# Kernel optimization log

Hardware: AMD Instinct MI355X
Metric: run time of the kernel (lower is better)

Reference implementation:

```python
import jax, jax.numpy as jnp
import numpy as np

B, C, P, H, W = 8, 256, 64, 64, 64


def conv2d(x, w, b, pad):
    y = jax.lax.conv_general_dilated(
        x, w, window_strides=(1, 1), padding=[(pad, pad), (pad, pad)],
        dimension_numbers=("NCHW", "OIHW", "NCHW"))
    return y + b[None, :, None, None]


def setup_inputs() -> dict:
    key = jax.random.key(0)
    ks = jax.random.split(key, 9)
    x = jax.random.normal(ks[0], (B, C, H, W), dtype=jnp.float32)
    # conv weights, OIHW layout; scale ~ kaiming-ish
    w_top = jax.random.normal(ks[1], (P, C, 1, 1), jnp.float32) * (1.0 / np.sqrt(C))
    b_top = jnp.zeros((P,), jnp.float32)
    w_center = jax.random.normal(ks[2], (P, C, 1, 1), jnp.float32) * (1.0 / np.sqrt(C))
    b_center = jnp.zeros((P,), jnp.float32)
    w_bottom = jax.random.normal(ks[3], (C, C, 3, 3), jnp.float32) * (1.0 / np.sqrt(9 * C))
    b_bottom = jnp.zeros((C,), jnp.float32)
    w_out = jax.random.normal(ks[4], (C, C, 3, 3), jnp.float32) * (1.0 / np.sqrt(9 * C))
    b_out = jnp.zeros((C,), jnp.float32)
    return {"x": x, "w_top": w_top, "b_top": b_top, "w_center": w_center,
            "b_center": b_center, "w_bottom": w_bottom, "b_bottom": b_bottom,
            "w_out": w_out, "b_out": b_out}


def reference(x, w_top, b_top, w_center, b_center, w_bottom, b_bottom, w_out, b_out):
    b, c, h, w = x.shape
    hw = h * w
    x_top = conv2d(x, w_top, b_top, 0).reshape(b, -1, hw)          # [B, P, HW]
    x_center = conv2d(x, w_center, b_center, 0).reshape(b, -1, hw)  # [B, P, HW]
    x_center = jnp.swapaxes(x_center, 1, 2)                          # [B, HW, P]
    x_bottom = conv2d(x, w_bottom, b_bottom, 1).reshape(b, c, hw)
    x_bottom = jnp.swapaxes(x_bottom, 1, 2)                          # [B, HW, C]
    sp_map = jnp.einsum("bnp,bpm->bnm", x_center, x_top)            # [B, HW, HW]
    # NOTE: softmax is GLOBAL over the flattened HW*HW map per batch element,
    # not per-row (faithful to original Softmax(dim=1) on view(bsize, -1)).
    sp_map = jax.nn.softmax(sp_map.reshape(b, -1), axis=1).reshape(b, hw, hw)
    sp_map = jnp.einsum("bnm,bmc->bnc", sp_map, x_bottom)           # [B, HW, C]
    # NOTE: original does .reshape(b, C, h, w) on a [B, HW, C] tensor (no
    # transpose) -- replicate that exact memory reinterpretation.
    sp_map = sp_map.reshape(b, c, h, w)
    return conv2d(x + sp_map, w_out, b_out, 1)
```

## Files before the change

kernel.cpp:

```cpp
#include <hip/hip_runtime.h>
#include <hip/hip_bf16.h>
#include <type_traits>

constexpr int B_ = 8, C_ = 256, P_ = 64, H_ = 64, W_ = 64, HW_ = 4096;

typedef __attribute__((ext_vector_type(8))) short short8;
typedef __attribute__((ext_vector_type(4))) short short4v;
typedef __attribute__((ext_vector_type(4))) float f32x4;

__device__ __forceinline__ short bfbits(float f) {
    __hip_bfloat16 h = __float2bfloat16(f);
    return *reinterpret_cast<short*>(&h);
}
__device__ __forceinline__ float bf2f(short s) {
    __hip_bfloat16 h = *reinterpret_cast<__hip_bfloat16*>(&s);
    return (float)h;
}

#define GLL16(gsrc, ldst)                                                      \
    __builtin_amdgcn_global_load_lds(                                         \
        (const __attribute__((address_space(1))) void*)(gsrc),                \
        (__attribute__((address_space(3))) void*)(ldst), 16, 0, 0)


__global__ __launch_bounds__(256) void k_prep_w(
    const float* __restrict__ w, short8* __restrict__ wbP)
{
    const int idx = blockIdx.x * 256 + threadIdx.x;
    const int lane = idx & 63, cot = (idx >> 6) & 15;
    const int cb = (idx >> 10) & 7, tap = idx >> 13;
    const int lm = lane & 15, lq = lane >> 4;
    const int co = cot * 16 + lm, ci0 = cb * 32 + lq * 8;
    short8 v;
#pragma unroll
    for (int k = 0; k < 8; ++k)
        v[k] = bfbits(w[(co * 256 + ci0 + k) * 9 + tap]);
    wbP[idx] = v;
}

__global__ __launch_bounds__(256) void k_prep_w1(
    const float* __restrict__ wt, const float* __restrict__ wc,
    short8* __restrict__ w1P)
{
    const int idx = blockIdx.x * 256 + threadIdx.x;
    const int lane = idx & 63, kc = (idx >> 6) & 7;
    const int pt = (idx >> 9) & 3, conv = idx >> 11;
    const int lm = lane & 15, lq = lane >> 4;
    const float* w = conv ? wc : wt;
    const float* wp = w + (pt * 16 + lm) * C_ + kc * 32 + lq * 8;
    short8 vh, vl;
#pragma unroll
    for (int k = 0; k < 8; ++k) {
        const float v = wp[k];
        const short h = bfbits(v);
        vh[k] = h;
        vl[k] = bfbits(v - bf2f(h));
    }
    const size_t o = (((size_t)(conv * 4 + pt) * 8 + kc) * 2) * 64 + lane;
    w1P[o] = vh;
    w1P[o + 64] = vl;
}

__global__ __launch_bounds__(256) void k_cvt_bf16(
    const float* __restrict__ x, short8* __restrict__ xB)
{
    const size_t i = ((size_t)blockIdx.x * 256 + threadIdx.x) * 16;
    short8 o[2];
#pragma unroll
    for (int q = 0; q < 2; ++q) {
#pragma unroll
        for (int j = 0; j < 2; ++j) {
            const float4 v = *reinterpret_cast<const float4*>(&x[i + q * 8 + j * 4]);
            o[q][j * 4 + 0] = bfbits(v.x);
            o[q][j * 4 + 1] = bfbits(v.y);
            o[q][j * 4 + 2] = bfbits(v.z);
            o[q][j * 4 + 3] = bfbits(v.w);
        }
    }
    short8* dp = (short8*)&xB[i >> 3];
    dp[0] = o[0];
    dp[1] = o[1];
}

__global__ __launch_bounds__(256) void k_pack_xb(
    const __hip_bfloat16* __restrict__ xb, short8* __restrict__ xbP)
{
    const int tid = blockIdx.x * 256 + threadIdx.x;
    const int lane = tid & 63, wid = tid >> 6;
    const int ct = wid & 15, g = (wid >> 4) & 127, b = wid >> 11;
    const int c = ct * 16 + (lane >> 2);
    const int mo = g * 32 + (lane & 3) * 8;
    const short8 v = *reinterpret_cast<const short8*>(
        &xb[((size_t)(b * 256 + c)) * HW_ + mo]);
    xbP[(size_t)wid * 64 + (lane & 3) * 16 + (lane >> 2)] = v;
}

__global__ __launch_bounds__(256) void k_conv1x1_mfma(
    const float* __restrict__ x, const short8* __restrict__ w1P,
    const float* __restrict__ b_top, const float* __restrict__ b_cen,
    short4v* __restrict__ xtPh, short4v* __restrict__ xtPl,
    short4v* __restrict__ xcPh, short4v* __restrict__ xcPl)
{
    const int b = blockIdx.y;
    const int t = threadIdx.x, wv = t >> 6, lane = t & 63;
    const int lm = lane & 15, lq = lane >> 4;
    const int nt = blockIdx.x * 4 + wv;
    const float* xp = x + (size_t)b * C_ * HW_ + nt * 16 + lm;

    f32x4 acc[2][4];
#pragma unroll
    for (int i = 0; i < 2; ++i)
#pragma unroll
        for (int j = 0; j < 4; ++j) acc[i][j] = f32x4{0.f, 0.f, 0.f, 0.f};

    for (int kc = 0; kc < 8; ++kc) {
        short8 bh, bl;
#pragma unroll
        for (int k = 0; k < 8; ++k) {
            const float v = xp[(size_t)(kc * 32 + lq * 8 + k) * HW_];
            const short h = bfbits(v);
            bh[k] = h;
            bl[k] = bfbits(v - bf2f(h));
        }
#pragma unroll
        for (int conv = 0; conv < 2; ++conv)
#pragma unroll
            for (int pt = 0; pt < 4; ++pt) {
                const size_t o =
                    (((size_t)(conv * 4 + pt) * 8 + kc) * 2) * 64 + lane;
                const short8 ah = w1P[o];
                const short8 al = w1P[o + 64];
                f32x4 a = acc[conv][pt];
                a = __builtin_amdgcn_mfma_f32_16x16x32_bf16(ah, bh, a, 0, 0, 0);
                a = __builtin_amdgcn_mfma_f32_16x16x32_bf16(ah, bl, a, 0, 0, 0);
                a = __builtin_amdgcn_mfma_f32_16x16x32_bf16(al, bh, a, 0, 0, 0);
                acc[conv][pt] = a;
            }
    }

#pragma unroll
    for (int conv = 0; conv < 2; ++conv) {
        const float* bias = conv ? b_cen : b_top;
        short4v* oh = conv ? xcPh : xtPh;
        short4v* ol = conv ? xcPl : xtPl;
#pragma unroll
        for (int pt = 0; pt < 4; ++pt) {
            const int kc = pt >> 1;
            const int tl = (pt & 1) * 2 + (lq >> 1);
            const size_t c16 = ((size_t)(b * 256 + nt) * 2 + kc) * 64 + tl * 16 + lm;
            short4v vh, vl;
#pragma unroll
            for (int r = 0; r < 4; ++r) {
                const float v = acc[conv][pt][r] + bias[pt * 16 + lq * 4 + r];
                const short h = bfbits(v);
                vh[r] = h;
                vl[r] = bfbits(v - bf2f(h));
            }
            oh[c16 * 2 + (lq & 1)] = vh;
            ol[c16 * 2 + (lq & 1)] = vl;
        }
    }
}

template <typename OT>
__global__ __launch_bounds__(1024, 4) void k_conv3x3_mfma(
    const short* __restrict__ xin, const short8* __restrict__ wbP,
    const float* __restrict__ bias, OT* __restrict__ out)
{
    __shared__ __align__(16) short Xs[4][66][40];
    const int lin = blockIdx.x;
    const int b = lin & 7, hp = lin >> 3;
    const int t = threadIdx.x;
    const int wave = t >> 6, lane = t & 63;
    const int lm = lane & 15, lq = lane >> 4;
    const int nq = wave >> 3, ch = wave & 7;

    f32x4 acc[4][2];
#pragma unroll
    for (int i = 0; i < 4; ++i)
#pragma unroll
        for (int j = 0; j < 2; ++j) acc[i][j] = f32x4{0.f, 0.f, 0.f, 0.f};

    if (t < 256) {
        const int r = t >> 6, cc = t & 31, side = (t >> 5) & 1;
        Xs[r][side ? 65 : 0][cc] = 0;
    }

    const short* xbase = xin + (size_t)b * C_ * HW_;

    for (int cb = 0; cb < 8; ++cb) {
        const int ci0 = cb * 32;
        __syncthreads();
#pragma unroll
        for (int it = 0; it < 2; ++it) {
            const int idx = it * 1024 + t;
            const int r = idx >> 9, ci = (idx >> 4) & 31, wq = idx & 15;
            const int hh = hp * 2 + r - 1;
            short4v v = {0, 0, 0, 0};
            if (hh >= 0 && hh < H_)
                v = *reinterpret_cast<const short4v*>(
                    &xbase[(size_t)(ci0 + ci) * HW_ + hh * W_ + wq * 4]);
            Xs[r][1 + wq * 4 + 0][ci] = v[0];
            Xs[r][1 + wq * 4 + 1][ci] = v[1];
            Xs[r][1 + wq * 4 + 2][ci] = v[2];
            Xs[r][1 + wq * 4 + 3][ci] = v[3];
        }
        __syncthreads();

#pragma unroll 3
        for (int tap = 0; tap < 9; ++tap) {
            const int dh = tap / 3;
            const int dw = tap % 3;
            const int slot = nq + dh;
            const short8* wp = wbP + ((size_t)(tap * 8 + cb)) * 1024 + lane;
            short8 af[2];
            af[0] = wp[(ch * 2 + 0) * 64];
            af[1] = wp[(ch * 2 + 1) * 64];
            short8 bf[4];
#pragma unroll
            for (int wt = 0; wt < 4; ++wt)
                bf[wt] = *reinterpret_cast<const short8*>(
                    &Xs[slot][wt * 16 + lm + dw][lq * 8]);
#pragma unroll
            for (int wt = 0; wt < 4; ++wt)
#pragma unroll
                for (int ct = 0; ct < 2; ++ct)
                    acc[wt][ct] = __builtin_amdgcn_mfma_f32_16x16x32_bf16(
                        af[ct], bf[wt], acc[wt][ct], 0, 0, 0);
        }
    }

#pragma unroll
    for (int wt = 0; wt < 4; ++wt) {
        const int pos = (hp * 2 + nq) * W_ + wt * 16 + lm;
#pragma unroll
        for (int ct = 0; ct < 2; ++ct) {
            const int co = ch * 32 + ct * 16 + lq * 4;
#pragma unroll
            for (int r = 0; r < 4; ++r) {
                const float v = acc[wt][ct][r] + bias[co + r];
                if constexpr (std::is_same<OT, __hip_bfloat16>::value)
                    out[((size_t)(b * C_ + co + r)) * HW_ + pos] = __float2bfloat16(v);
                else
                    out[((size_t)(b * C_ + co + r)) * HW_ + pos] = v;
            }
        }
    }
}

__global__ __launch_bounds__(512, 2) void k_attn_mfma(
    const short8* __restrict__ xtPh, const short8* __restrict__ xtPl,
    const short8* __restrict__ xcPh, const short8* __restrict__ xcPl,
    const short8* __restrict__ xbP, float* __restrict__ O,
    float* __restrict__ Z)
{
    extern __shared__ __align__(16) char smem[];
    short8* XTs = (short8*)smem;
    short8* XBs = (short8*)(smem + 32768);
    short8* Ps8 = (short8*)(smem + 98304);
    short4v* Ps4 = (short4v*)(smem + 98304);
    float* zred = (float*)(smem + 114688);

    const int lin = blockIdx.x;
    const int b = lin & 7, nblk = lin >> 3;
    const int n0 = nblk * 128;

    const int t = threadIdx.x, wv = t >> 6, lane = t & 63;
    const int lm = lane & 15, lq = lane >> 4;
    const int mh = wv >> 2, nq2 = wv & 3;
    const int nq = wv >> 2, cq = wv & 3;

    short8 cB2[2][2][2];
#pragma unroll
    for (int ntile = 0; ntile < 2; ++ntile) {
        const int gt = nblk * 8 + nq2 * 2 + ntile;
        const size_t base = ((size_t)(b * 256 + gt) * 2) * 64 + lane;
        cB2[ntile][0][0] = xcPh[base];
        cB2[ntile][1][0] = xcPh[base + 64];
        cB2[ntile][0][1] = xcPl[base];
        cB2[ntile][1][1] = xcPl[base + 64];
    }
    asm volatile("s_waitcnt vmcnt(0)" ::: "memory");

    auto stage = [&](int smt, int bufi) {
        short8* XT = XTs + bufi * 1024;
        short8* XB = XBs + bufi * 2048;
        const size_t abase = ((size_t)(b * 512 + smt * 8)) * 64;
#pragma unroll
        for (int k = 0; k < 2; ++k) {
            const int c = wv * 2 + k, ms = c >> 2, part = c & 3;
            const short8* src = (part < 2 ? xtPh : xtPl)
                                + abase + ms * 128 + (part & 1) * 64 + lane;
            GLL16(src, XT + c * 64);
        }
        const size_t p8 = ((size_t)(b * 2048 + smt * 32)) * 64;
#pragma unroll
        for (int k = 0; k < 4; ++k) {
            const int e = k * 512 + wv * 64;
            GLL16(xbP + p8 + e + lane, XB + e);
        }
    };
    stage(0, 0);

    f32x4 acc[4][4];
#pragma unroll
    for (int i = 0; i < 4; ++i)
#pragma unroll
        for (int jj = 0; jj < 4; ++jj) acc[i][jj] = f32x4{0.f, 0.f, 0.f, 0.f};
    float zp = 0.f;

    for (int mt = 0; mt < 64; ++mt) {
        const int cur = mt & 1;
        asm volatile("s_waitcnt vmcnt(4)" ::: "memory");
        __builtin_amdgcn_sched_barrier(0);
        __builtin_amdgcn_s_barrier();
        __builtin_amdgcn_sched_barrier(0);
        stage((mt + 1) & 63, cur ^ 1);

        const short8* XT = XTs + cur * 1024;
#pragma unroll
        for (int ms2 = 0; ms2 < 2; ++ms2) {
            const int ms = mh * 2 + ms2;
            const short8 aH0 = XT[(ms * 4 + 0) * 64 + lane];
            const short8 aH1 = XT[(ms * 4 + 1) * 64 + lane];
            const short8 aL0 = XT[(ms * 4 + 2) * 64 + lane];
            const short8 aL1 = XT[(ms * 4 + 3) * 64 + lane];
#pragma unroll
            for (int ntile = 0; ntile < 2; ++ntile) {
                f32x4 s = {0.f, 0.f, 0.f, 0.f};
                __builtin_amdgcn_s_setprio(1);
                s = __builtin_amdgcn_mfma_f32_16x16x32_bf16(aH0, cB2[ntile][0][0], s, 0, 0, 0);
                s = __builtin_amdgcn_mfma_f32_16x16x32_bf16(aH1, cB2[ntile][1][0], s, 0, 0, 0);
                s = __builtin_amdgcn_mfma_f32_16x16x32_bf16(aH0, cB2[ntile][0][1], s, 0, 0, 0);
                s = __builtin_amdgcn_mfma_f32_16x16x32_bf16(aH1, cB2[ntile][1][1], s, 0, 0, 0);
                s = __builtin_amdgcn_mfma_f32_16x16x32_bf16(aL0, cB2[ntile][0][0], s, 0, 0, 0);
                s = __builtin_amdgcn_mfma_f32_16x16x32_bf16(aL1, cB2[ntile][1][0], s, 0, 0, 0);
                __builtin_amdgcn_s_setprio(0);
                const float e0 = __expf(s[0]), e1 = __expf(s[1]);
                const float e2 = __expf(s[2]), e3 = __expf(s[3]);
                zp += (e0 + e1) + (e2 + e3);
                short4v pk = { bfbits(e0), bfbits(e1), bfbits(e2), bfbits(e3) };
                const int T = nq2 * 2 + ntile;
                const int lqp = (ms & 1) * 2 + (lq >> 1);
                Ps4[(((T * 2 + mh) * 64) + lqp * 16 + lm) * 2 + (lq & 1)] = pk;
            }
        }
        asm volatile("s_waitcnt vmcnt(6) lgkmcnt(0)" ::: "memory");
        __builtin_amdgcn_sched_barrier(0);
        __builtin_amdgcn_s_barrier();
        __builtin_amdgcn_sched_barrier(0);

        const short8* XB = XBs + cur * 2048;
        short8 vb0[4], vb1[4];
#pragma unroll
        for (int q4 = 0; q4 < 4; ++q4) {
            const int ct = cq * 4 + q4;
            vb0[q4] = XB[ct * 64 + lane];
            vb1[q4] = XB[1024 + ct * 64 + lane];
        }
#pragma unroll
        for (int nt2 = 0; nt2 < 4; ++nt2) {
            const int T = nq * 4 + nt2;
            const short8 pa0 = Ps8[(T * 2 + 0) * 64 + lane];
            const short8 pa1 = Ps8[(T * 2 + 1) * 64 + lane];
            __builtin_amdgcn_s_setprio(1);
#pragma unroll
            for (int q4 = 0; q4 < 4; ++q4) {
                acc[nt2][q4] = __builtin_amdgcn_mfma_f32_16x16x32_bf16(
                    pa0, vb0[q4], acc[nt2][q4], 0, 0, 0);
                acc[nt2][q4] = __builtin_amdgcn_mfma_f32_16x16x32_bf16(
                    pa1, vb1[q4], acc[nt2][q4], 0, 0, 0);
            }
            __builtin_amdgcn_s_setprio(0);
        }
    }

#pragma unroll
    for (int o = 32; o > 0; o >>= 1) zp += __shfl_down(zp, o, 64);
    if (lane == 0) zred[wv] = zp;
    __syncthreads();
    if (t == 0) {
        float zs = 0.f;
#pragma unroll
        for (int wvi = 0; wvi < 8; ++wvi) zs += zred[wvi];
        atomicAdd(&Z[b], zs);
    }

#pragma unroll
    for (int nt2 = 0; nt2 < 4; ++nt2) {
#pragma unroll
        for (int q4 = 0; q4 < 4; ++q4) {
            const int c = cq * 64 + q4 * 16 + lm;
#pragma unroll
            for (int r = 0; r < 4; ++r) {
                const int n = n0 + (nq * 4 + nt2) * 16 + lq * 4 + r;
                O[((size_t)b * HW_ + n) * C_ + c] = acc[nt2][q4][r];
            }
        }
    }
}

__global__ __launch_bounds__(256) void k_add_bf16(
    const float* __restrict__ x, const float* __restrict__ o,
    const float* __restrict__ Z, short4v* __restrict__ yB)
{
    const int bidx = blockIdx.x;
    const float invZ = 1.0f / Z[bidx >> 10];
    const size_t i = ((size_t)bidx * 256 + threadIdx.x) * 4;
    const float4 a = *reinterpret_cast<const float4*>(&x[i]);
    const float4 b = *reinterpret_cast<const float4*>(&o[i]);
    short4v r{bfbits(fmaf(b.x, invZ, a.x)), bfbits(fmaf(b.y, invZ, a.y)),
              bfbits(fmaf(b.z, invZ, a.z)), bfbits(fmaf(b.w, invZ, a.w))};
    yB[i >> 2] = r;
}

extern "C" void kernel_launch(void* const* d_in, const int* in_sizes, int n_in,
                              void* d_out, int out_size, void* d_ws, size_t ws_size,
                              hipStream_t stream)
{
    const float* x   = (const float*)d_in[0];
    const float* wt  = (const float*)d_in[1];
    const float* bt  = (const float*)d_in[2];
    const float* wc  = (const float*)d_in[3];
    const float* bc  = (const float*)d_in[4];
    const float* wbo = (const float*)d_in[5];
    const float* bbo = (const float*)d_in[6];
    const float* wo  = (const float*)d_in[7];
    const float* bo  = (const float*)d_in[8];
    float* out = (float*)d_out;

    uint8_t* w8 = (uint8_t*)d_ws;
    const size_t MB = 1u << 20;
    short8* xtPh = (short8*)(w8);
    short8* xtPl = (short8*)(w8 + 4 * MB);
    short8* xcPh = (short8*)(w8 + 8 * MB);
    short8* xcPl = (short8*)(w8 + 12 * MB);
    short8* W1   = (short8*)(w8 + 16 * MB);
    __hip_bfloat16* xbB = (__hip_bfloat16*)(w8 + 16 * MB);
    short8* xbP  = (short8*)(w8 + 32 * MB);
    float*  O    = (float*)(w8 + 48 * MB);
    short8* Wb1  = (short8*)(w8 + 48 * MB);
    short8* xB   = (short8*)(w8 + 64 * MB);
    short8* Wb2  = (short8*)(w8 + 32 * MB);
    short4v* yB  = (short4v*)(w8 + 16 * MB);
    float*  Z    = (float*)(w8 + 80 * MB);

    hipMemsetAsync(Z, 0, B_ * sizeof(float), stream);
    k_prep_w<<<dim3(288), 256, 0, stream>>>(wbo, Wb1);
    k_prep_w1<<<dim3(16), 256, 0, stream>>>(wt, wc, W1);
    k_cvt_bf16<<<dim3(2048), 256, 0, stream>>>(x, xB);
    k_conv1x1_mfma<<<dim3(64, 8), 256, 0, stream>>>(
        x, W1, bt, bc, (short4v*)xtPh, (short4v*)xtPl,
        (short4v*)xcPh, (short4v*)xcPl);
    k_conv3x3_mfma<__hip_bfloat16><<<dim3(256), 1024, 0, stream>>>(
        (const short*)xB, Wb1, bbo, xbB);
    k_pack_xb<<<dim3(4096), 256, 0, stream>>>(xbB, xbP);
    k_attn_mfma<<<dim3(256), dim3(512), 114720, stream>>>(xtPh, xtPl, xcPh, xcPl,
                                                          xbP, O, Z);
    k_prep_w<<<dim3(288), 256, 0, stream>>>(wo, Wb2);
    k_add_bf16<<<dim3(8192), 256, 0, stream>>>(x, O, Z, yB);
    k_conv3x3_mfma<float><<<dim3(256), 1024, 0, stream>>>(
        (const short*)yB, Wb2, bo, out);
}
```

Before: 362.0 us.

## Software-pipeline attention loop: overlap next tile's score MFMAs with current PV

Restructures the attention main loop so the QK score/exp computation for tile mt+1 is interleaved with the P·V MFMAs for tile mt. The P buffer is double-buffered in LDS, which grows shared memory to about 128KB. XT loads are prefetched two tiles ahead and XB loads one tile ahead, and one of the two barriers per iteration is removed. The goal is to hide the exp and VALU latency behind MFMA work and cut barrier stalls. In exchange, the larger LDS footprint may reduce occupancy, and register pressure rises.

```diff
diff --git a/kernel.cpp b/kernel.cpp
--- a/kernel.cpp
+++ b/kernel.cpp
@@ -259,7 +259,7 @@
     short8* XBs = (short8*)(smem + 32768);
     short8* Ps8 = (short8*)(smem + 98304);
     short4v* Ps4 = (short4v*)(smem + 98304);
-    float* zred = (float*)(smem + 114688);
+    float* zred = (float*)(smem + 131072);
 
     const int lin = blockIdx.x;
     const int b = lin & 7, nblk = lin >> 3;
@@ -282,25 +282,26 @@
     }
     asm volatile("s_waitcnt vmcnt(0)" ::: "memory");
 
-    auto stage = [&](int smt, int bufi) {
-        short8* XT = XTs + bufi * 1024;
-        short8* XB = XBs + bufi * 2048;
-        const size_t abase = ((size_t)(b * 512 + smt * 8)) * 64;
-#pragma unroll
-        for (int k = 0; k < 2; ++k) {
-            const int c = wv * 2 + k, ms = c >> 2, part = c & 3;
+    auto stageXT = [&](int k) {
+        short8* XT = XTs + (k & 1) * 1024;
+        const size_t abase = ((size_t)(b * 512 + k * 8)) * 64;
+#pragma unroll
+        for (int j = 0; j < 2; ++j) {
+            const int c = wv * 2 + j, ms = c >> 2, part = c & 3;
             const short8* src = (part < 2 ? xtPh : xtPl)
                                 + abase + ms * 128 + (part & 1) * 64 + lane;
             GLL16(src, XT + c * 64);
         }
-        const size_t p8 = ((size_t)(b * 2048 + smt * 32)) * 64;
-#pragma unroll
-        for (int k = 0; k < 4; ++k) {
-            const int e = k * 512 + wv * 64;
+    };
+    auto stageXB = [&](int k) {
+        short8* XB = XBs + (k & 1) * 2048;
+        const size_t p8 = ((size_t)(b * 2048 + k * 32)) * 64;
+#pragma unroll
+        for (int j = 0; j < 4; ++j) {
+            const int e = j * 512 + wv * 64;
             GLL16(xbP + p8 + e + lane, XB + e);
         }
     };
-    stage(0, 0);
 
     f32x4 acc[4][4];
 #pragma unroll
@@ -309,48 +310,70 @@
         for (int jj = 0; jj < 4; ++jj) acc[i][jj] = f32x4{0.f, 0.f, 0.f, 0.f};
     float zp = 0.f;
 
-    for (int mt = 0; mt < 64; ++mt) {
-        const int cur = mt & 1;
-        asm volatile("s_waitcnt vmcnt(4)" ::: "memory");
+    auto st_slice = [&](int k, int i) {
+        const short8* XT = XTs + (k & 1) * 1024;
+        const int stb = (k & 1) * 2048;
+        const int ms2 = i >> 1, ntile = i & 1;
+        const int ms = mh * 2 + ms2;
+        const short8 aH0 = XT[(ms * 4 + 0) * 64 + lane];
+        const short8 aH1 = XT[(ms * 4 + 1) * 64 + lane];
+        const short8 aL0 = XT[(ms * 4 + 2) * 64 + lane];
+        const short8 aL1 = XT[(ms * 4 + 3) * 64 + lane];
+        f32x4 s = {0.f, 0.f, 0.f, 0.f};
+        __builtin_amdgcn_s_setprio(1);
+        s = __builtin_amdgcn_mfma_f32_16x16x32_bf16(aH0, cB2[ntile][0][0], s, 0, 0, 0);
+        s = __builtin_amdgcn_mfma_f32_16x16x32_bf16(aH1, cB2[ntile][1][0], s, 0, 0, 0);
+        s = __builtin_amdgcn_mfma_f32_16x16x32_bf16(aH0, cB2[ntile][0][1], s, 0, 0, 0);
+        s = __builtin_amdgcn_mfma_f32_16x16x32_bf16(aH1, cB2[ntile][1][1], s, 0, 0, 0);
+        s = __builtin_amdgcn_mfma_f32_16x16x32_bf16(aL0, cB2[ntile][0][0], s, 0, 0, 0);
+        s = __builtin_amdgcn_mfma_f32_16x16x32_bf16(aL1, cB2[ntile][1][0], s, 0, 0, 0);
+        __builtin_amdgcn_s_setprio(0);
+        const float e0 = __expf(s[0]), e1 = __expf(s[1]);
+        const float e2 = __expf(s[2]), e3 = __expf(s[3]);
+        zp += (e0 + e1) + (e2 + e3);
+        short4v pk = { bfbits(e0), bfbits(e1), bfbits(e2), bfbits(e3) };
+        const int T = nq2 * 2 + ntile;
+        const int lqp = (ms & 1) * 2 + (lq >> 1);
+        Ps4[stb + (((T * 2 + mh) * 64) + lqp * 16 + lm) * 2 + (lq & 1)] = pk;
+    };
+
+    auto pv_chunk = [&](int mt, int nt2, const short8* vb0, const short8* vb1) {
+        const int pvb = (mt & 1) * 1024;
+        const int T = nq * 4 + nt2;
+        const short8 pa0 = Ps8[pvb + (T * 2 + 0) * 64 + lane];
+        const short8 pa1 = Ps8[pvb + (T * 2 + 1) * 64 + lane];
+        __builtin_amdgcn_s_setprio(1);
+#pragma unroll
+        for (int q4 = 0; q4 < 4; ++q4) {
+            acc[nt2][q4] = __builtin_amdgcn_mfma_f32_16x16x32_bf16(
+                pa0, vb0[q4], acc[nt2][q4], 0, 0, 0);
+            acc[nt2][q4] = __builtin_amdgcn_mfma_f32_16x16x32_bf16(
+                pa1, vb1[q4], acc[nt2][q4], 0, 0, 0);
+        }
+        __builtin_amdgcn_s_setprio(0);
+    };
+
+    stageXT(0);
+    stageXB(0);
+    stageXT(1);
+    asm volatile("s_waitcnt vmcnt(2)" ::: "memory");
+    __builtin_amdgcn_sched_barrier(0);
+    __builtin_amdgcn_s_barrier();
+    __builtin_amdgcn_sched_barrier(0);
+#pragma unroll
+    for (int i = 0; i < 4; ++i) st_slice(0, i);
+    asm volatile("s_waitcnt lgkmcnt(0)" ::: "memory");
+    __builtin_amdgcn_sched_barrier(0);
+
+    for (int mt = 0; mt < 63; ++mt) {
+        asm volatile("s_waitcnt vmcnt(0)" ::: "memory");
         __builtin_amdgcn_sched_barrier(0);
         __builtin_amdgcn_s_barrier();
         __builtin_amdgcn_sched_barrier(0);
-        stage((mt + 1) & 63, cur ^ 1);
-
-        const short8* XT = XTs + cur * 1024;
-#pragma unroll
-        for (int ms2 = 0; ms2 < 2; ++ms2) {
-            const int ms = mh * 2 + ms2;
-            const short8 aH0 = XT[(ms * 4 + 0) * 64 + lane];
-            const short8 aH1 = XT[(ms * 4 + 1) * 64 + lane];
-            const short8 aL0 = XT[(ms * 4 + 2) * 64 + lane];
-            const short8 aL1 = XT[(ms * 4 + 3) * 64 + lane];
-#pragma unroll
-            for (int ntile = 0; ntile < 2; ++ntile) {
-                f32x4 s = {0.f, 0.f, 0.f, 0.f};
-                __builtin_amdgcn_s_setprio(1);
-                s = __builtin_amdgcn_mfma_f32_16x16x32_bf16(aH0, cB2[ntile][0][0], s, 0, 0, 0);
-                s = __builtin_amdgcn_mfma_f32_16x16x32_bf16(aH1, cB2[ntile][1][0], s, 0, 0, 0);
-                s = __builtin_amdgcn_mfma_f32_16x16x32_bf16(aH0, cB2[ntile][0][1], s, 0, 0, 0);
-                s = __builtin_amdgcn_mfma_f32_16x16x32_bf16(aH1, cB2[ntile][1][1], s, 0, 0, 0);
-                s = __builtin_amdgcn_mfma_f32_16x16x32_bf16(aL0, cB2[ntile][0][0], s, 0, 0, 0);
-                s = __builtin_amdgcn_mfma_f32_16x16x32_bf16(aL1, cB2[ntile][1][0], s, 0, 0, 0);
-                __builtin_amdgcn_s_setprio(0);
-                const float e0 = __expf(s[0]), e1 = __expf(s[1]);
-                const float e2 = __expf(s[2]), e3 = __expf(s[3]);
-                zp += (e0 + e1) + (e2 + e3);
-                short4v pk = { bfbits(e0), bfbits(e1), bfbits(e2), bfbits(e3) };
-                const int T = nq2 * 2 + ntile;
-                const int lqp = (ms & 1) * 2 + (lq >> 1);
-                Ps4[(((T * 2 + mh) * 64) + lqp * 16 + lm) * 2 + (lq & 1)] = pk;
-            }
-        }
-        asm volatile("s_waitcnt vmcnt(6) lgkmcnt(0)" ::: "memory");
-        __builtin_amdgcn_sched_barrier(0);
-        __builtin_amdgcn_s_barrier();
-        __builtin_amdgcn_sched_barrier(0);
-
-        const short8* XB = XBs + cur * 2048;
+        stageXB(mt + 1);
+        if (mt < 62) stageXT(mt + 2);
+
+        const short8* XB = XBs + (mt & 1) * 2048;
         short8 vb0[4], vb1[4];
 #pragma unroll
         for (int q4 = 0; q4 < 4; ++q4) {
@@ -359,20 +382,29 @@
             vb1[q4] = XB[1024 + ct * 64 + lane];
         }
 #pragma unroll
-        for (int nt2 = 0; nt2 < 4; ++nt2) {
-            const int T = nq * 4 + nt2;
-            const short8 pa0 = Ps8[(T * 2 + 0) * 64 + lane];
-            const short8 pa1 = Ps8[(T * 2 + 1) * 64 + lane];
-            __builtin_amdgcn_s_setprio(1);
-#pragma unroll
-            for (int q4 = 0; q4 < 4; ++q4) {
-                acc[nt2][q4] = __builtin_amdgcn_mfma_f32_16x16x32_bf16(
-                    pa0, vb0[q4], acc[nt2][q4], 0, 0, 0);
-                acc[nt2][q4] = __builtin_amdgcn_mfma_f32_16x16x32_bf16(
-                    pa1, vb1[q4], acc[nt2][q4], 0, 0, 0);
-            }
-            __builtin_amdgcn_s_setprio(0);
-        }
+        for (int i = 0; i < 4; ++i) {
+            st_slice(mt + 1, i);
+            pv_chunk(mt, i, vb0, vb1);
+        }
+        asm volatile("s_waitcnt lgkmcnt(0)" ::: "memory");
+        __builtin_amdgcn_sched_barrier(0);
+    }
+
+    asm volatile("s_waitcnt vmcnt(0)" ::: "memory");
+    __builtin_amdgcn_sched_barrier(0);
+    __builtin_amdgcn_s_barrier();
+    __builtin_amdgcn_sched_barrier(0);
+    {
+        const short8* XB = XBs + (63 & 1) * 2048;
+        short8 vb0[4], vb1[4];
+#pragma unroll
+        for (int q4 = 0; q4 < 4; ++q4) {
+            const int ct = cq * 4 + q4;
+            vb0[q4] = XB[ct * 64 + lane];
+            vb1[q4] = XB[1024 + ct * 64 + lane];
+        }
+#pragma unroll
+        for (int i = 0; i < 4; ++i) pv_chunk(63, i, vb0, vb1);
     }
 
 #pragma unroll
@@ -455,7 +487,7 @@
     k_conv3x3_mfma<__hip_bfloat16><<<dim3(256), 1024, 0, stream>>>(
         (const short*)xB, Wb1, bbo, xbB);
     k_pack_xb<<<dim3(4096), 256, 0, stream>>>(xbB, xbP);
-    k_attn_mfma<<<dim3(256), dim3(512), 114720, stream>>>(xtPh, xtPl, xcPh, xcPl,
+    k_attn_mfma<<<dim3(256), dim3(512), 131104, stream>>>(xtPh, xtPl, xcPh, xcPl,
                                                           xbP, O, Z);
     k_prep_w<<<dim3(288), 256, 0, stream>>>(wo, Wb2);
     k_add_bf16<<<dim3(8192), 256, 0, stream>>>(x, O, Z, yB);
```

Measured after the change: 363.6 us. About the same (+0.4%).

## Double attention kernel block to 16 waves, halving per-wave tile work

Applied to the files above, without the earlier changes.

The attention kernel now launches 1024 threads per block instead of 512. Each wave handles one score tile instead of two, and half as many output channel tiles. Staging loads are redistributed across 16 waves, and the wait counts and Z reduction are adjusted to match. The goal is more waves per CU to hide MFMA and LDS latency and to reduce register pressure. The cost is more barrier participants and, with over 114KB of shared memory, likely still only one block per CU, so the launch_bounds occupancy hint of 4 is unreachable.

```diff
diff --git a/kernel.cpp b/kernel.cpp
--- a/kernel.cpp
+++ b/kernel.cpp
@@ -248,7 +248,7 @@
     }
 }
 
-__global__ __launch_bounds__(512, 2) void k_attn_mfma(
+__global__ __launch_bounds__(1024, 4) void k_attn_mfma(
     const short8* __restrict__ xtPh, const short8* __restrict__ xtPl,
     const short8* __restrict__ xcPh, const short8* __restrict__ xcPl,
     const short8* __restrict__ xbP, float* __restrict__ O,
@@ -267,18 +267,17 @@
 
     const int t = threadIdx.x, wv = t >> 6, lane = t & 63;
     const int lm = lane & 15, lq = lane >> 4;
-    const int mh = wv >> 2, nq2 = wv & 3;
-    const int nq = wv >> 2, cq = wv & 3;
-
-    short8 cB2[2][2][2];
-#pragma unroll
-    for (int ntile = 0; ntile < 2; ++ntile) {
-        const int gt = nblk * 8 + nq2 * 2 + ntile;
+    const int mh = wv >> 3, nq2 = wv & 7;
+    const int nq = wv >> 3, cq = wv & 7;
+
+    short8 cB2[2][2];
+    {
+        const int gt = nblk * 8 + nq2;
         const size_t base = ((size_t)(b * 256 + gt) * 2) * 64 + lane;
-        cB2[ntile][0][0] = xcPh[base];
-        cB2[ntile][1][0] = xcPh[base + 64];
-        cB2[ntile][0][1] = xcPl[base];
-        cB2[ntile][1][1] = xcPl[base + 64];
+        cB2[0][0] = xcPh[base];
+        cB2[1][0] = xcPh[base + 64];
+        cB2[0][1] = xcPl[base];
+        cB2[1][1] = xcPl[base + 64];
     }
     asm volatile("s_waitcnt vmcnt(0)" ::: "memory");
 
@@ -286,32 +285,31 @@
         short8* XT = XTs + bufi * 1024;
         short8* XB = XBs + bufi * 2048;
         const size_t abase = ((size_t)(b * 512 + smt * 8)) * 64;
-#pragma unroll
-        for (int k = 0; k < 2; ++k) {
-            const int c = wv * 2 + k, ms = c >> 2, part = c & 3;
+        {
+            const int c = wv, ms = c >> 2, part = c & 3;
             const short8* src = (part < 2 ? xtPh : xtPl)
                                 + abase + ms * 128 + (part & 1) * 64 + lane;
             GLL16(src, XT + c * 64);
         }
         const size_t p8 = ((size_t)(b * 2048 + smt * 32)) * 64;
 #pragma unroll
-        for (int k = 0; k < 4; ++k) {
-            const int e = k * 512 + wv * 64;
+        for (int j = 0; j < 2; ++j) {
+            const int e = (wv * 2 + j) * 64;
             GLL16(xbP + p8 + e + lane, XB + e);
         }
     };
     stage(0, 0);
 
-    f32x4 acc[4][4];
+    f32x4 acc[4][2];
 #pragma unroll
     for (int i = 0; i < 4; ++i)
 #pragma unroll
-        for (int jj = 0; jj < 4; ++jj) acc[i][jj] = f32x4{0.f, 0.f, 0.f, 0.f};
+        for (int jj = 0; jj < 2; ++jj) acc[i][jj] = f32x4{0.f, 0.f, 0.f, 0.f};
     float zp = 0.f;
 
     for (int mt = 0; mt < 64; ++mt) {
         const int cur = mt & 1;
-        asm volatile("s_waitcnt vmcnt(4)" ::: "memory");
+        asm volatile("s_waitcnt vmcnt(2)" ::: "memory");
         __builtin_amdgcn_sched_barrier(0);
         __builtin_amdgcn_s_barrier();
         __builtin_amdgcn_sched_barrier(0);
@@ -325,38 +323,35 @@
             const short8 aH1 = XT[(ms * 4 + 1) * 64 + lane];
             const short8 aL0 = XT[(ms * 4 + 2) * 64 + lane];
             const short8 aL1 = XT[(ms * 4 + 3) * 64 + lane];
-#pragma unroll
-            for (int ntile = 0; ntile < 2; ++ntile) {
-                f32x4 s = {0.f, 0.f, 0.f, 0.f};
-                __builtin_amdgcn_s_setprio(1);
-                s = __builtin_amdgcn_mfma_f32_16x16x32_bf16(aH0, cB2[ntile][0][0], s, 0, 0, 0);
-                s = __builtin_amdgcn_mfma_f32_16x16x32_bf16(aH1, cB2[ntile][1][0], s, 0, 0, 0);
-                s = __builtin_amdgcn_mfma_f32_16x16x32_bf16(aH0, cB2[ntile][0][1], s, 0, 0, 0);
-                s = __builtin_amdgcn_mfma_f32_16x16x32_bf16(aH1, cB2[ntile][1][1], s, 0, 0, 0);
-                s = __builtin_amdgcn_mfma_f32_16x16x32_bf16(aL0, cB2[ntile][0][0], s, 0, 0, 0);
-                s = __builtin_amdgcn_mfma_f32_16x16x32_bf16(aL1, cB2[ntile][1][0], s, 0, 0, 0);
-                __builtin_amdgcn_s_setprio(0);
-                const float e0 = __expf(s[0]), e1 = __expf(s[1]);
-                const float e2 = __expf(s[2]), e3 = __expf(s[3]);
-                zp += (e0 + e1) + (e2 + e3);
-                short4v pk = { bfbits(e0), bfbits(e1), bfbits(e2), bfbits(e3) };
-                const int T = nq2 * 2 + ntile;
-                const int lqp = (ms & 1) * 2 + (lq >> 1);
-                Ps4[(((T * 2 + mh) * 64) + lqp * 16 + lm) * 2 + (lq & 1)] = pk;
-            }
-        }
-        asm volatile("s_waitcnt vmcnt(6) lgkmcnt(0)" ::: "memory");
+            f32x4 s = {0.f, 0.f, 0.f, 0.f};
+            __builtin_amdgcn_s_setprio(1);
+            s = __builtin_amdgcn_mfma_f32_16x16x32_bf16(aH0, cB2[0][0], s, 0, 0, 0);
+            s = __builtin_amdgcn_mfma_f32_16x16x32_bf16(aH1, cB2[1][0], s, 0, 0, 0);
+            s = __builtin_amdgcn_mfma_f32_16x16x32_bf16(aH0, cB2[0][1], s, 0, 0, 0);
+            s = __builtin_amdgcn_mfma_f32_16x16x32_bf16(aH1, cB2[1][1], s, 0, 0, 0);
+            s = __builtin_amdgcn_mfma_f32_16x16x32_bf16(aL0, cB2[0][0], s, 0, 0, 0);
+            s = __builtin_amdgcn_mfma_f32_16x16x32_bf16(aL1, cB2[1][0], s, 0, 0, 0);
+            __builtin_amdgcn_s_setprio(0);
+            const float e0 = __expf(s[0]), e1 = __expf(s[1]);
+            const float e2 = __expf(s[2]), e3 = __expf(s[3]);
+            zp += (e0 + e1) + (e2 + e3);
+            short4v pk = { bfbits(e0), bfbits(e1), bfbits(e2), bfbits(e3) };
+            const int T = nq2;
+            const int lqp = ms2 * 2 + (lq >> 1);
+            Ps4[(((T * 2 + mh) * 64) + lqp * 16 + lm) * 2 + (lq & 1)] = pk;
+        }
+        asm volatile("s_waitcnt vmcnt(3) lgkmcnt(0)" ::: "memory");
         __builtin_amdgcn_sched_barrier(0);
         __builtin_amdgcn_s_barrier();
         __builtin_amdgcn_sched_barrier(0);
 
         const short8* XB = XBs + cur * 2048;
-        short8 vb0[4], vb1[4];
-#pragma unroll
-        for (int q4 = 0; q4 < 4; ++q4) {
-            const int ct = cq * 4 + q4;
-            vb0[q4] = XB[ct * 64 + lane];
-            vb1[q4] = XB[1024 + ct * 64 + lane];
+        short8 vb0[2], vb1[2];
+#pragma unroll
+        for (int q2 = 0; q2 < 2; ++q2) {
+            const int ct = cq * 2 + q2;
+            vb0[q2] = XB[ct * 64 + lane];
+            vb1[q2] = XB[1024 + ct * 64 + lane];
         }
 #pragma unroll
         for (int nt2 = 0; nt2 < 4; ++nt2) {
@@ -365,11 +360,11 @@
             const short8 pa1 = Ps8[(T * 2 + 1) * 64 + lane];
             __builtin_amdgcn_s_setprio(1);
 #pragma unroll
-            for (int q4 = 0; q4 < 4; ++q4) {
-                acc[nt2][q4] = __builtin_amdgcn_mfma_f32_16x16x32_bf16(
-                    pa0, vb0[q4], acc[nt2][q4], 0, 0, 0);
-                acc[nt2][q4] = __builtin_amdgcn_mfma_f32_16x16x32_bf16(
-                    pa1, vb1[q4], acc[nt2][q4], 0, 0, 0);
+            for (int q2 = 0; q2 < 2; ++q2) {
+                acc[nt2][q2] = __builtin_amdgcn_mfma_f32_16x16x32_bf16(
+                    pa0, vb0[q2], acc[nt2][q2], 0, 0, 0);
+                acc[nt2][q2] = __builtin_amdgcn_mfma_f32_16x16x32_bf16(
+                    pa1, vb1[q2], acc[nt2][q2], 0, 0, 0);
             }
             __builtin_amdgcn_s_setprio(0);
         }
@@ -382,19 +377,19 @@
     if (t == 0) {
         float zs = 0.f;
 #pragma unroll
-        for (int wvi = 0; wvi < 8; ++wvi) zs += zred[wvi];
+        for (int wvi = 0; wvi < 16; ++wvi) zs += zred[wvi];
         atomicAdd(&Z[b], zs);
     }
 
 #pragma unroll
     for (int nt2 = 0; nt2 < 4; ++nt2) {
 #pragma unroll
-        for (int q4 = 0; q4 < 4; ++q4) {
-            const int c = cq * 64 + q4 * 16 + lm;
+        for (int q2 = 0; q2 < 2; ++q2) {
+            const int c = cq * 32 + q2 * 16 + lm;
 #pragma unroll
             for (int r = 0; r < 4; ++r) {
                 const int n = n0 + (nq * 4 + nt2) * 16 + lq * 4 + r;
-                O[((size_t)b * HW_ + n) * C_ + c] = acc[nt2][q4][r];
+                O[((size_t)b * HW_ + n) * C_ + c] = acc[nt2][q2][r];
             }
         }
     }
@@ -455,8 +450,8 @@
     k_conv3x3_mfma<__hip_bfloat16><<<dim3(256), 1024, 0, stream>>>(
         (const short*)xB, Wb1, bbo, xbB);
     k_pack_xb<<<dim3(4096), 256, 0, stream>>>(xbB, xbP);
-    k_attn_mfma<<<dim3(256), dim3(512), 114720, stream>>>(xtPh, xtPl, xcPh, xcPl,
-                                                          xbP, O, Z);
+    k_attn_mfma<<<dim3(256), dim3(1024), 114752, stream>>>(xtPh, xtPl, xcPh, xcPl,
+                                                           xbP, O, Z);
     k_prep_w<<<dim3(288), 256, 0, stream>>>(wo, Wb2);
     k_add_bf16<<<dim3(8192), 256, 0, stream>>>(x, O, Z, yB);
     k_conv3x3_mfma<float><<<dim3(256), 1024, 0, stream>>>(
```

Result: no change. 365.0 us (+0.8%).
